# Performance work log

Hardware: AMD Instinct MI355X
Metric: run time of the kernel (lower is better)

Reference implementation:

```python
import jax, jax.numpy as jnp
import numpy as np

N_NODES = 100000
N_EDGES = 6400000
GAIN_BASE = 10.0


def setup_inputs() -> dict:
    key = jax.random.key(0)
    ks = jax.random.split(key, 9)
    rates = jax.random.normal(ks[0], (N_NODES,), dtype=jnp.float32)
    weights = jax.random.normal(ks[1], (N_EDGES,), dtype=jnp.float32) * 0.1
    gain = jax.random.uniform(ks[2], (N_NODES,), dtype=jnp.float32) * 0.5  # gain_base**gain stays moderate
    time_constant = jax.random.uniform(ks[3], (N_NODES,), dtype=jnp.float32) + 0.5  # in [0.5, 1.5]
    baseline = jax.random.normal(ks[4], (N_NODES,), dtype=jnp.float32) * 0.1
    ext_input = jax.random.normal(ks[5], (N_NODES,), dtype=jnp.float32)
    src = jax.random.randint(ks[6], (N_EDGES,), 0, N_NODES, dtype=jnp.int32)
    dst = jax.random.randint(ks[7], (N_EDGES,), 0, N_NODES, dtype=jnp.int32)
    is_input = jax.random.randint(ks[8], (N_NODES,), 0, 2) > 0
    return {
        "rates": rates, "weights": weights, "gain": gain,
        "time_constant": time_constant, "baseline": baseline,
        "ext_input": ext_input, "src": src, "dst": dst, "is_input": is_input,
    }


def reference(rates, weights, gain, time_constant, baseline, ext_input, src, dst, is_input):
    # synaptic_input[v] = sum over incoming edges (u->v) of rates[u] * weight(u,v)
    messages = rates[src] * weights                      # [E] gather + multiply
    syn = jax.ops.segment_sum(messages, dst, num_segments=N_NODES)  # [N]
    # input nodes get external input only; others get synaptic input
    total = jnp.where(is_input, ext_input, syn) + baseline
    act = jnp.tanh(total)
    # dr/dt = (1/tau) * (-r + gain_base**gain * activation(input))
    return (-rates + jnp.power(GAIN_BASE, gain) * act) / time_constant
```

## Files before the change

### kernel.cpp

```cpp
#include <hip/hip_runtime.h>
#include <math.h>

#define N_NODES 100000
#define N_EDGES 6400000
#define K_BINS  5
#define BIN_SZ  20000
#define BLOCK   1024
#define LOG2_10 3.321928094887362f

__global__ __launch_bounds__(BLOCK) void edge_bin_kernel(
        const float* __restrict__ rates,
        const float* __restrict__ weights,
        const int* __restrict__ src,
        const int* __restrict__ dst,
        float* __restrict__ part,
        int n_chunks, int edges_per_chunk) {
    __shared__ float bin[BIN_SZ];
    const int b = blockIdx.x % K_BINS;
    const int c = blockIdx.x / K_BINS;
    const int base_node = b * BIN_SZ;

    for (int i = threadIdx.x; i < BIN_SZ; i += BLOCK) bin[i] = 0.0f;
    __syncthreads();

    const long e0 = (long)c * edges_per_chunk;
    const int nvec = edges_per_chunk >> 2;
    const int4*   s4 = (const int4*)(src + e0);
    const int4*   d4 = (const int4*)(dst + e0);
    const float4* w4 = (const float4*)(weights + e0);

    for (int i = threadIdx.x; i < nvec; i += BLOCK) {
        int4   d = d4[i];
        int4   s = s4[i];
        float4 w = w4[i];
        unsigned dx = (unsigned)(d.x - base_node);
        unsigned dy = (unsigned)(d.y - base_node);
        unsigned dz = (unsigned)(d.z - base_node);
        unsigned dw = (unsigned)(d.w - base_node);
        if (dx < BIN_SZ) atomicAdd(&bin[dx], rates[s.x] * w.x);
        if (dy < BIN_SZ) atomicAdd(&bin[dy], rates[s.y] * w.y);
        if (dz < BIN_SZ) atomicAdd(&bin[dz], rates[s.z] * w.z);
        if (dw < BIN_SZ) atomicAdd(&bin[dw], rates[s.w] * w.w);
    }
    __syncthreads();

    float4* outp = (float4*)(part + (size_t)c * N_NODES + base_node);
    for (int i = threadIdx.x; i < (BIN_SZ >> 2); i += BLOCK) {
        outp[i] = make_float4(bin[4*i], bin[4*i+1], bin[4*i+2], bin[4*i+3]);
    }
}

__global__ void node_kernel(const float* __restrict__ rates,
                            const float* __restrict__ gain,
                            const float* __restrict__ time_constant,
                            const float* __restrict__ baseline,
                            const float* __restrict__ ext_input,
                            const int*   __restrict__ is_input,
                            const float* __restrict__ part,
                            float* __restrict__ out,
                            int n_chunks) {
    int v = blockIdx.x * blockDim.x + threadIdx.x;
    if (v >= N_NODES) return;
    float s0 = 0.0f, s1 = 0.0f, s2 = 0.0f, s3 = 0.0f;
    int k = 0;
    for (; k + 3 < n_chunks; k += 4) {
        s0 += part[(size_t)(k + 0) * N_NODES + v];
        s1 += part[(size_t)(k + 1) * N_NODES + v];
        s2 += part[(size_t)(k + 2) * N_NODES + v];
        s3 += part[(size_t)(k + 3) * N_NODES + v];
    }
    for (; k < n_chunks; ++k) s0 += part[(size_t)k * N_NODES + v];
    float s = (s0 + s1) + (s2 + s3);
    float total = (is_input[v] != 0 ? ext_input[v] : s) + baseline[v];
    float act = tanhf(total);
    float g = exp2f(gain[v] * LOG2_10);
    out[v] = (-rates[v] + g * act) / time_constant[v];
}

extern "C" void kernel_launch(void* const* d_in, const int* in_sizes, int n_in,
                              void* d_out, int out_size, void* d_ws, size_t ws_size,
                              hipStream_t stream) {
    const float* rates         = (const float*)d_in[0];
    const float* weights       = (const float*)d_in[1];
    const float* gain          = (const float*)d_in[2];
    const float* time_constant = (const float*)d_in[3];
    const float* baseline      = (const float*)d_in[4];
    const float* ext_input     = (const float*)d_in[5];
    const int*   src           = (const int*)d_in[6];
    const int*   dst           = (const int*)d_in[7];
    const int*   is_input      = (const int*)d_in[8];
    float* out  = (float*)d_out;
    float* part = (float*)d_ws;

    static const int cand[] = {100, 50, 25, 20, 10, 5, 4, 2, 1};
    int n_chunks = 1;
    for (int i = 0; i < (int)(sizeof(cand)/sizeof(cand[0])); ++i) {
        if ((size_t)cand[i] * N_NODES * sizeof(float) <= ws_size) { n_chunks = cand[i]; break; }
    }
    int edges_per_chunk = N_EDGES / n_chunks;

    int grid_e = K_BINS * n_chunks;
    edge_bin_kernel<<<grid_e, BLOCK, 0, stream>>>(rates, weights, src, dst,
                                                  part, n_chunks, edges_per_chunk);

    int block = 256;
    int grid_n = (N_NODES + block - 1) / block;
    node_kernel<<<grid_n, block, 0, stream>>>(rates, gain, time_constant, baseline,
                                              ext_input, is_input, part, out, n_chunks);
}
```

Measured before the change: 188.8 us.

## Replace multi-pass LDS binning with single-pass global atomics into replicated bins

Edges are now streamed once and scattered with global atomic adds into 8 replicated node-sized accumulators (chosen by block index), instead of re-reading all edges once per LDS bin. The node kernel sums the 8 copies and processes four nodes per thread with vector loads. This removes the repeated edge-array reads but relies on L2 atomic throughput and contention, and adds a memset of the accumulators. It also assumes the workspace holds 8 node arrays without checking ws_size.

Measured after the change: 421.4 us. 123% more time.

```diff
diff --git a/kernel.cpp b/kernel.cpp
--- a/kernel.cpp
+++ b/kernel.cpp
@@ -3,50 +3,32 @@
 
 #define N_NODES 100000
 #define N_EDGES 6400000
-#define K_BINS  5
-#define BIN_SZ  20000
-#define BLOCK   1024
+#define NCOPY   8
+#define EBLOCK  256
+#define EGRID   2048
 #define LOG2_10 3.321928094887362f
 
-__global__ __launch_bounds__(BLOCK) void edge_bin_kernel(
+__global__ __launch_bounds__(EBLOCK) void edge_scatter_kernel(
         const float* __restrict__ rates,
         const float* __restrict__ weights,
         const int* __restrict__ src,
         const int* __restrict__ dst,
-        float* __restrict__ part,
-        int n_chunks, int edges_per_chunk) {
-    __shared__ float bin[BIN_SZ];
-    const int b = blockIdx.x % K_BINS;
-    const int c = blockIdx.x / K_BINS;
-    const int base_node = b * BIN_SZ;
-
-    for (int i = threadIdx.x; i < BIN_SZ; i += BLOCK) bin[i] = 0.0f;
-    __syncthreads();
-
-    const long e0 = (long)c * edges_per_chunk;
-    const int nvec = edges_per_chunk >> 2;
-    const int4*   s4 = (const int4*)(src + e0);
-    const int4*   d4 = (const int4*)(dst + e0);
-    const float4* w4 = (const float4*)(weights + e0);
-
-    for (int i = threadIdx.x; i < nvec; i += BLOCK) {
+        float* __restrict__ part) {
+    float* mybin = part + (size_t)(blockIdx.x & (NCOPY - 1)) * N_NODES;
+    const int nq = N_EDGES >> 2;
+    const int4*   s4 = (const int4*)src;
+    const int4*   d4 = (const int4*)dst;
+    const float4* w4 = (const float4*)weights;
+    const int stride = gridDim.x * blockDim.x;
+    for (int i = blockIdx.x * blockDim.x + threadIdx.x; i < nq; i += stride) {
         int4   d = d4[i];
         int4   s = s4[i];
         float4 w = w4[i];
-        unsigned dx = (unsigned)(d.x - base_node);
-        unsigned dy = (unsigned)(d.y - base_node);
-        unsigned dz = (unsigned)(d.z - base_node);
-        unsigned dw = (unsigned)(d.w - base_node);
-        if (dx < BIN_SZ) atomicAdd(&bin[dx], rates[s.x] * w.x);
-        if (dy < BIN_SZ) atomicAdd(&bin[dy], rates[s.y] * w.y);
-        if (dz < BIN_SZ) atomicAdd(&bin[dz], rates[s.z] * w.z);
-        if (dw < BIN_SZ) atomicAdd(&bin[dw], rates[s.w] * w.w);
-    }
-    __syncthreads();
-
-    float4* outp = (float4*)(part + (size_t)c * N_NODES + base_node);
-    for (int i = threadIdx.x; i < (BIN_SZ >> 2); i += BLOCK) {
-        outp[i] = make_float4(bin[4*i], bin[4*i+1], bin[4*i+2], bin[4*i+3]);
+        float rx = rates[s.x], ry = rates[s.y], rz = rates[s.z], rw = rates[s.w];
+        atomicAdd(&mybin[d.x], rx * w.x);
+        atomicAdd(&mybin[d.y], ry * w.y);
+        atomicAdd(&mybin[d.z], rz * w.z);
+        atomicAdd(&mybin[d.w], rw * w.w);
     }
 }
 
@@ -57,24 +39,37 @@
                             const float* __restrict__ ext_input,
                             const int*   __restrict__ is_input,
                             const float* __restrict__ part,
-                            float* __restrict__ out,
-                            int n_chunks) {
-    int v = blockIdx.x * blockDim.x + threadIdx.x;
-    if (v >= N_NODES) return;
-    float s0 = 0.0f, s1 = 0.0f, s2 = 0.0f, s3 = 0.0f;
-    int k = 0;
-    for (; k + 3 < n_chunks; k += 4) {
-        s0 += part[(size_t)(k + 0) * N_NODES + v];
-        s1 += part[(size_t)(k + 1) * N_NODES + v];
-        s2 += part[(size_t)(k + 2) * N_NODES + v];
-        s3 += part[(size_t)(k + 3) * N_NODES + v];
-    }
-    for (; k < n_chunks; ++k) s0 += part[(size_t)k * N_NODES + v];
-    float s = (s0 + s1) + (s2 + s3);
-    float total = (is_input[v] != 0 ? ext_input[v] : s) + baseline[v];
-    float act = tanhf(total);
-    float g = exp2f(gain[v] * LOG2_10);
-    out[v] = (-rates[v] + g * act) / time_constant[v];
+                            float* __restrict__ out) {
+    const int t = blockIdx.x * blockDim.x + threadIdx.x;
+    if (t >= (N_NODES >> 2)) return;
+
+    float4 p0 = ((const float4*)(part + 0 * (size_t)N_NODES))[t];
+    float4 p1 = ((const float4*)(part + 1 * (size_t)N_NODES))[t];
+    float4 p2 = ((const float4*)(part + 2 * (size_t)N_NODES))[t];
+    float4 p3 = ((const float4*)(part + 3 * (size_t)N_NODES))[t];
+    float4 p4 = ((const float4*)(part + 4 * (size_t)N_NODES))[t];
+    float4 p5 = ((const float4*)(part + 5 * (size_t)N_NODES))[t];
+    float4 p6 = ((const float4*)(part + 6 * (size_t)N_NODES))[t];
+    float4 p7 = ((const float4*)(part + 7 * (size_t)N_NODES))[t];
+
+    float4 r   = ((const float4*)rates)[t];
+    float4 g   = ((const float4*)gain)[t];
+    float4 tc  = ((const float4*)time_constant)[t];
+    float4 bl  = ((const float4*)baseline)[t];
+    float4 ext = ((const float4*)ext_input)[t];
+    int4   ii  = ((const int4*)is_input)[t];
+
+    float sx = ((p0.x + p1.x) + (p2.x + p3.x)) + ((p4.x + p5.x) + (p6.x + p7.x));
+    float sy = ((p0.y + p1.y) + (p2.y + p3.y)) + ((p4.y + p5.y) + (p6.y + p7.y));
+    float sz = ((p0.z + p1.z) + (p2.z + p3.z)) + ((p4.z + p5.z) + (p6.z + p7.z));
+    float sw = ((p0.w + p1.w) + (p2.w + p3.w)) + ((p4.w + p5.w) + (p6.w + p7.w));
+
+    float4 o;
+    o.x = (-r.x + exp2f(g.x * LOG2_10) * tanhf((ii.x ? ext.x : sx) + bl.x)) / tc.x;
+    o.y = (-r.y + exp2f(g.y * LOG2_10) * tanhf((ii.y ? ext.y : sy) + bl.y)) / tc.y;
+    o.z = (-r.z + exp2f(g.z * LOG2_10) * tanhf((ii.z ? ext.z : sz) + bl.z)) / tc.z;
+    o.w = (-r.w + exp2f(g.w * LOG2_10) * tanhf((ii.w ? ext.w : sw) + bl.w)) / tc.w;
+    ((float4*)out)[t] = o;
 }
 
 extern "C" void kernel_launch(void* const* d_in, const int* in_sizes, int n_in,
@@ -92,19 +87,12 @@
     float* out  = (float*)d_out;
     float* part = (float*)d_ws;
 
-    static const int cand[] = {100, 50, 25, 20, 10, 5, 4, 2, 1};
-    int n_chunks = 1;
-    for (int i = 0; i < (int)(sizeof(cand)/sizeof(cand[0])); ++i) {
-        if ((size_t)cand[i] * N_NODES * sizeof(float) <= ws_size) { n_chunks = cand[i]; break; }
-    }
-    int edges_per_chunk = N_EDGES / n_chunks;
+    hipMemsetAsync(part, 0, (size_t)NCOPY * N_NODES * sizeof(float), stream);
 
-    int grid_e = K_BINS * n_chunks;
-    edge_bin_kernel<<<grid_e, BLOCK, 0, stream>>>(rates, weights, src, dst,
-                                                  part, n_chunks, edges_per_chunk);
+    edge_scatter_kernel<<<EGRID, EBLOCK, 0, stream>>>(rates, weights, src, dst, part);
 
     int block = 256;
-    int grid_n = (N_NODES + block - 1) / block;
+    int grid_n = ((N_NODES >> 2) + block - 1) / block;
     node_kernel<<<grid_n, block, 0, stream>>>(rates, gain, time_constant, baseline,
-                                              ext_input, is_input, part, out, n_chunks);
+                                              ext_input, is_input, part, out);
 }
```
